# Kernel tuning notes

Measured on AMD Instinct MI355X. Metric: run time of the kernel, lower is better.

The kernel has to match this reference:

```python
import jax, jax.numpy as jnp
import numpy as np

EPS = 1e-5

def gru_step(x, h, Wih, Whh, bih, bhh):
    # PyTorch GRU cell math. x:[B,C], h:[B,H], Wih:[3H,C], Whh:[3H,H]
    gi = x @ Wih.T + bih
    gh = h @ Whh.T + bhh
    ir, iz, inn = jnp.split(gi, 3, axis=-1)
    hr, hz, hn = jnp.split(gh, 3, axis=-1)
    r = jax.nn.sigmoid(ir + hr)
    z = jax.nn.sigmoid(iz + hz)
    n = jnp.tanh(inn + r * hn)
    return (1.0 - z) * n + z * h

def batchnorm_train(x, g, b):
    # x:[B,C]; training-mode BN over batch dim, biased variance
    mu = jnp.mean(x, axis=0)
    var = jnp.mean((x - mu) ** 2, axis=0)
    return g * (x - mu) / jnp.sqrt(var + EPS) + b

def setup_inputs() -> dict:
    B, Le, T = 256, 1024, 48
    Fe, Fd, G, R, H = 16, 16, 32, 16, 256
    Ce, Cd = Fe + R, Fd + R + 1  # 32, 33
    key = jax.random.key(0)
    ks = jax.random.split(key, 24)
    s = 0.05
    inp = {
        "X_Encoder": jax.random.normal(ks[0], (B, Le, Fe), jnp.float32),
        "X_Decoder": jax.random.normal(ks[1], (B, T, Fd), jnp.float32),
        "Xg_Encoder": jax.random.normal(ks[2], (B, Le, G), jnp.float32),
        "Xg_Decoder": jax.random.normal(ks[3], (B, T, G), jnp.float32),
        # global feature reducers
        "Wg_enc": jax.random.normal(ks[4], (R, G), jnp.float32) * s,
        "bg_enc": jnp.zeros((R,), jnp.float32),
        "Wg_dec": jax.random.normal(ks[5], (R, G), jnp.float32) * s,
        "bg_dec": jnp.zeros((R,), jnp.float32),
        # encoder GRU + output head
        "enc_Wih": jax.random.normal(ks[6], (3 * H, Ce), jnp.float32) * s,
        "enc_Whh": jax.random.normal(ks[7], (3 * H, H), jnp.float32) * s,
        "enc_bih": jnp.zeros((3 * H,), jnp.float32),
        "enc_bhh": jnp.zeros((3 * H,), jnp.float32),
        "enc_Wo": jax.random.normal(ks[8], (1, H), jnp.float32) * s,
        "enc_bo": jnp.zeros((1,), jnp.float32),
        # decoder GRU + output head
        "dec_Wih": jax.random.normal(ks[9], (3 * H, Cd), jnp.float32) * s,
        "dec_Whh": jax.random.normal(ks[10], (3 * H, H), jnp.float32) * s,
        "dec_bih": jnp.zeros((3 * H,), jnp.float32),
        "dec_bhh": jnp.zeros((3 * H,), jnp.float32),
        "dec_Wo": jax.random.normal(ks[11], (1, H), jnp.float32) * s,
        "dec_bo": jnp.zeros((1,), jnp.float32),
        # BatchNorm params: BN_1 and per-step BN_layers (T of them)
        "bn1_g": jnp.ones((Cd,), jnp.float32),
        "bn1_b": jnp.zeros((Cd,), jnp.float32),
        "bnT_g": jnp.ones((T, Cd), jnp.float32),
        "bnT_b": jnp.zeros((T, Cd), jnp.float32),
    }
    return inp

def reference(X_Encoder, X_Decoder, Xg_Encoder, Xg_Decoder,
              Wg_enc, bg_enc, Wg_dec, bg_dec,
              enc_Wih, enc_Whh, enc_bih, enc_bhh, enc_Wo, enc_bo,
              dec_Wih, dec_Whh, dec_bih, dec_bhh, dec_Wo, dec_bo,
              bn1_g, bn1_b, bnT_g, bnT_b):
    B, Le, _ = X_Encoder.shape
    T = X_Decoder.shape[1]
    H = enc_Whh.shape[1]
    # batched global-feature reduction (replaces nested per-element loops)
    enc_in = jnp.concatenate([X_Encoder, Xg_Encoder @ Wg_enc.T + bg_enc], axis=2)  # [B,Le,Ce]
    dec_wg = jnp.concatenate([X_Decoder, Xg_Decoder @ Wg_dec.T + bg_dec], axis=2)  # [B,T,Fd+R]
    # encoder: sequential GRU over Le steps
    def estep(h, x):
        return gru_step(x, h, enc_Wih, enc_Whh, enc_bih, enc_bhh), None
    h0 = jnp.zeros((B, H), enc_in.dtype)
    h_enc, _ = jax.lax.scan(estep, h0, jnp.swapaxes(enc_in, 0, 1))
    enc_out = h_enc @ enc_Wo.T + enc_bo  # [B,1]
    # first decoder input: concat + BN_1 (train mode); dropout p=0 -> identity
    dec_in0 = batchnorm_train(jnp.concatenate([dec_wg[:, 0], enc_out], axis=1), bn1_g, bn1_b)
    # next-step exogenous inputs, padded with zeros for the (unused) last step
    next_x = jnp.concatenate([dec_wg[:, 1:], jnp.zeros((B, 1, dec_wg.shape[2]), dec_wg.dtype)], axis=1)
    next_x = jnp.swapaxes(next_x, 0, 1)  # [T,B,Fd+R]
    def dstep(carry, xs):
        h, dinp = carry
        nx, g, b = xs
        h = gru_step(dinp, h, dec_Wih, dec_Whh, dec_bih, dec_bhh)
        out = h @ dec_Wo.T + dec_bo  # [B,1]
        new_in = batchnorm_train(jnp.concatenate([nx, out], axis=1), g, b)
        return (h, new_in), out
    (_, _), outs = jax.lax.scan(dstep, (h_enc, dec_in0), (next_x, bnT_g, bnT_b))
    return jnp.swapaxes(outs, 0, 1)  # [B,T,1]
```

## Files before the change

### kernel.cpp

```cpp
#include <hip/hip_runtime.h>
#include <math.h>

typedef _Float16 f16;
typedef _Float16 f16x8 __attribute__((ext_vector_type(8)));
typedef float f32x4 __attribute__((ext_vector_type(4)));

#define MFMA16(A_, B_, C_) __builtin_amdgcn_mfma_f32_16x16x32_f16((A_), (B_), (C_), 0, 0, 0)

__device__ __forceinline__ float sigf(float x) { return 1.0f / (1.0f + __expf(-x)); }
__device__ __forceinline__ float tanhf_(float x) { float e = __expf(2.0f * x); return 1.0f - 2.0f / (e + 1.0f); }

static const size_t OFF_ENCIN = 0;
static const size_t OFF_DECIN = 16777216;
static const size_t OFF_WENC  = OFF_DECIN + 786432;
static const size_t OFF_WDEC  = OFF_WENC + 442368;
static const size_t OFF_W32   = OFF_WDEC + 442368;
static const size_t OFF_BE    = OFF_W32 + 3072;
static const size_t OFF_BD    = OFF_BE + 4096;
static const size_t OFF_HENC  = OFF_BD + 4096;
static const size_t OFF_EOUT  = OFF_HENC + 131072;
static const size_t OFF_XST   = OFF_EOUT + 1024;
static const size_t OFF_OST   = OFF_XST + 12288;
static const size_t OFF_BAR   = OFF_OST + 512;

struct P {
  const float *Xe, *Xd, *Xge, *Xgd, *Wge, *bge, *Wgd, *bgd;
  const float *eWih, *eWhh, *ebih, *ebhh, *eWo, *ebo;
  const float *dWih, *dWhh, *dbih, *dbhh, *dWo, *dbo;
  const float *bn1g, *bn1b, *bnTg, *bnTb;
  f16 *encin, *decin, *wencf, *wdecf;
  float *w32, *bE, *bD;
  f16 *henc;
  float *eout, *xst, *ost;
  int *bar;
  float *out;
};

__global__ void prep1(P p) {
  const int blk = blockIdx.x, tid = threadIdx.x;
  __shared__ float swg[512];
  __shared__ float sbg[16];
  if (blk < 1024) {
    for (int i = tid; i < 512; i += 256) swg[i] = p.Wge[i];
    if (tid < 16) sbg[tid] = p.bge[tid];
    __syncthreads();
    const int i = blk * 256 + tid;
    const int b = i >> 10, t = i & 1023;
    const float* xg = p.Xge + (size_t)(b * 1024 + t) * 32;
    const float* xe = p.Xe + (size_t)(b * 1024 + t) * 16;
    f16* o = p.encin + (size_t)(t * 256 + b) * 32;
    float xgv[32];
#pragma unroll
    for (int k = 0; k < 32; ++k) xgv[k] = xg[k];
#pragma unroll
    for (int c = 0; c < 16; ++c) o[c] = (f16)xe[c];
#pragma unroll 4
    for (int r = 0; r < 16; ++r) {
      float acc = sbg[r];
#pragma unroll
      for (int k = 0; k < 32; ++k) acc += swg[r * 32 + k] * xgv[k];
      o[16 + r] = (f16)acc;
    }
  } else if (blk < 1072) {
    for (int i = tid; i < 512; i += 256) swg[i] = p.Wgd[i];
    if (tid < 16) sbg[tid] = p.bgd[tid];
    __syncthreads();
    const int i = (blk - 1024) * 256 + tid;
    const int b = i / 48, t = i - b * 48;
    const float* xg = p.Xgd + (size_t)(b * 48 + t) * 32;
    const float* xd = p.Xd + (size_t)(b * 48 + t) * 16;
    f16* o = p.decin + (size_t)(t * 256 + b) * 32;
    float xgv[32];
#pragma unroll
    for (int k = 0; k < 32; ++k) xgv[k] = xg[k];
#pragma unroll
    for (int c = 0; c < 16; ++c) o[c] = (f16)xd[c];
#pragma unroll 4
    for (int r = 0; r < 16; ++r) {
      float acc = sbg[r];
#pragma unroll
      for (int k = 0; k < 32; ++k) acc += swg[r * 32 + k] * xgv[k];
      o[16 + r] = (f16)acc;
    }
  } else if (blk < 1180) {
    const int i = (blk - 1072) * 256 + tid;
    const int kt = i / 3072, r2 = i - kt * 3072;
    const int nt = r2 >> 6, l = r2 & 63;
    const int n = nt * 16 + (l & 15), g = l >> 4;
    f16* o = p.wencf + (size_t)i * 8;
#pragma unroll
    for (int j = 0; j < 8; ++j) {
      const int k = g * 8 + j;
      o[j] = (f16)((kt == 0) ? p.eWih[n * 32 + k] : p.eWhh[n * 256 + (kt - 1) * 32 + k]);
    }
  } else if (blk < 1288) {
    const int i = (blk - 1180) * 256 + tid;
    const int kt = i / 3072, r2 = i - kt * 3072;
    const int nt = r2 >> 6, l = r2 & 63;
    const int n = nt * 16 + (l & 15), g = l >> 4;
    f16* o = p.wdecf + (size_t)i * 8;
#pragma unroll
    for (int j = 0; j < 8; ++j) {
      const int k = g * 8 + j;
      o[j] = (f16)((kt == 0) ? p.dWih[n * 33 + k] : p.dWhh[n * 256 + (kt - 1) * 32 + k]);
    }
  } else if (blk == 1288) {
    for (int i = tid; i < 768; i += 256) p.w32[i] = p.dWih[i * 33 + 32];
    for (int i = tid; i < 96; i += 256) p.ost[i] = 0.f;
    if (tid == 0) { p.bar[0] = 0; p.bar[1] = 0; }
  } else if (blk == 1289) {
    for (int i = tid; i < 1024; i += 256) {
      float v;
      if (i < 512) v = p.ebih[i] + p.ebhh[i];
      else if (i < 768) v = p.ebih[i];
      else v = p.ebhh[i - 256];
      p.bE[i] = v;
    }
  } else {
    for (int i = tid; i < 1024; i += 256) {
      float v;
      if (i < 512) v = p.dbih[i] + p.dbhh[i];
      else if (i < 768) v = p.dbih[i];
      else v = p.dbhh[i - 256];
      p.bD[i] = v;
    }
  }
}

__global__ void prep2(P p) {
  const int i = blockIdx.x * 256 + threadIdx.x;
  if (i >= 48 * 32) return;
  const int s = i >> 5, c = i & 31;
  float s1 = 0.f, s2 = 0.f;
  for (int b = 0; b < 256; ++b) {
    const float v = (float)p.decin[(size_t)(s * 256 + b) * 32 + c];
    s1 += v; s2 += v * v;
  }
  const float mu = s1 * (1.0f / 256.0f);
  p.xst[i * 2] = mu;
  p.xst[i * 2 + 1] = s2 * (1.0f / 256.0f) - mu * mu;
}

__device__ __forceinline__ void gridbar(int* bar) {
  __syncthreads();
  if (threadIdx.x == 0) {
    const int g = __hip_atomic_load(&bar[1], __ATOMIC_ACQUIRE, __HIP_MEMORY_SCOPE_AGENT);
    const int a = __hip_atomic_fetch_add(&bar[0], 1, __ATOMIC_ACQ_REL, __HIP_MEMORY_SCOPE_AGENT);
    if (a == 15) {
      __hip_atomic_store(&bar[0], 0, __ATOMIC_RELAXED, __HIP_MEMORY_SCOPE_AGENT);
      __hip_atomic_store(&bar[1], g + 1, __ATOMIC_RELEASE, __HIP_MEMORY_SCOPE_AGENT);
    } else {
      while (__hip_atomic_load(&bar[1], __ATOMIC_ACQUIRE, __HIP_MEMORY_SCOPE_AGENT) == g) {
        __builtin_amdgcn_s_sleep(2);
      }
    }
  }
  __syncthreads();
}

__global__ __launch_bounds__(512, 2) void enc_kernel(P p) {
  __shared__ f16 sWL[49152];
  __shared__ f16 sH[8192];
  __shared__ float sRed[512];
  const int tid = threadIdx.x;
  const int l = tid & 63, w = tid >> 6;
  const int g = l >> 4, m16 = l & 15;
  const int sw16 = (m16 & 7) << 4;
  const int bg = blockIdx.x * 16;

  {
    const int4* src = (const int4*)(p.wencf + 172032);
    int4* dst = (int4*)sWL;
#pragma unroll
    for (int i = 0; i < 12; ++i) dst[tid + i * 512] = src[tid + i * 512];
  }
  {
    int* hz = (int*)sH;
#pragma unroll
    for (int i = 0; i < 8; ++i) hz[tid + i * 512] = 0;
  }
  const int nts[6] = {w, 8 + w, 16 + w, 24 + w, 32 + w, 40 + w};
  f16x8 Wr[7][6];
#pragma unroll
  for (int kt = 0; kt < 7; ++kt)
#pragma unroll
    for (int i = 0; i < 6; ++i)
      Wr[kt][i] = *(const f16x8*)(p.wencf + ((size_t)(kt * 48 + nts[i]) * 64 + l) * 8);
  const int J1 = 16 * w + m16, J2 = 128 + J1;
  const float br1 = p.bE[J1], bz1 = p.bE[256 + J1], bi1 = p.bE[512 + J1], bh1 = p.bE[768 + J1];
  const float br2 = p.bE[J2], bz2 = p.bE[256 + J2], bi2 = p.bE[512 + J2], bh2 = p.bE[768 + J2];
  __syncthreads();

  int ph = 0;
  f16x8 xf = *(const f16x8*)(p.encin + (size_t)(bg + m16) * 32 + 8 * g);
#pragma unroll 1
  for (int t = 0; t < 1024; ++t) {
    const int tn = (t < 1023) ? t + 1 : t;
    const f16x8 xn = *(const f16x8*)(p.encin + (size_t)(tn * 256 + bg + m16) * 32 + 8 * g);
    f32x4 aR0 = {0,0,0,0}, aR1 = {0,0,0,0}, aZ0 = {0,0,0,0}, aZ1 = {0,0,0,0};
    f32x4 aNi0 = {0,0,0,0}, aNi1 = {0,0,0,0}, aNh0 = {0,0,0,0}, aNh1 = {0,0,0,0};
    aR0 = MFMA16(xf, Wr[0][0], aR0);
    aR1 = MFMA16(xf, Wr[0][1], aR1);
    aZ0 = MFMA16(xf, Wr[0][2], aZ0);
    aZ1 = MFMA16(xf, Wr[0][3], aZ1);
    aNi0 = MFMA16(xf, Wr[0][4], aNi0);
    aNi1 = MFMA16(xf, Wr[0][5], aNi1);
#pragma unroll
    for (int kk = 1; kk <= 6; ++kk) {
      const f16x8 a = *(const f16x8*)((const char*)sH + ph * 8192 + m16 * 512 +
                                      ((64 * (kk - 1) + 16 * g) ^ sw16));
      aR0 = MFMA16(a, Wr[kk][0], aR0);
      aR1 = MFMA16(a, Wr[kk][1], aR1);
      aZ0 = MFMA16(a, Wr[kk][2], aZ0);
      aZ1 = MFMA16(a, Wr[kk][3], aZ1);
      aNh0 = MFMA16(a, Wr[kk][4], aNh0);
      aNh1 = MFMA16(a, Wr[kk][5], aNh1);
    }
#pragma unroll
    for (int kk = 7; kk <= 8; ++kk) {
      const f16x8 a = *(const f16x8*)((const char*)sH + ph * 8192 + m16 * 512 +
                                      ((64 * (kk - 1) + 16 * g) ^ sw16));
      const char* wb = (const char*)sWL + (kk - 7) * 49152;
      const f16x8 q0 = *(const f16x8*)(wb + (nts[0] * 64 + l) * 16);
      const f16x8 q1 = *(const f16x8*)(wb + (nts[1] * 64 + l) * 16);
      const f16x8 q2 = *(const f16x8*)(wb + (nts[2] * 64 + l) * 16);
      const f16x8 q3 = *(const f16x8*)(wb + (nts[3] * 64 + l) * 16);
      const f16x8 q4 = *(const f16x8*)(wb + (nts[4] * 64 + l) * 16);
      const f16x8 q5 = *(const f16x8*)(wb + (nts[5] * 64 + l) * 16);
      aR0 = MFMA16(a, q0, aR0);
      aR1 = MFMA16(a, q1, aR1);
      aZ0 = MFMA16(a, q2, aZ0);
      aZ1 = MFMA16(a, q3, aZ1);
      aNh0 = MFMA16(a, q4, aNh0);
      aNh1 = MFMA16(a, q5, aNh1);
    }
    {
      char* hw = (char*)sH + (ph ^ 1) * 8192;
      const char* hr = (const char*)sH + ph * 8192;
#pragma unroll
      for (int q = 0; q < 4; ++q) {
        const int m = 4 * g + q;
        const int sw = (m & 7) << 4;
        const float h1 = (float)*(const f16*)(hr + m * 512 + ((2 * J1) ^ sw));
        const float r1 = sigf(aR0[q] + br1);
        const float z1 = sigf(aZ0[q] + bz1);
        const float n1 = tanhf_(aNi0[q] + bi1 + r1 * (aNh0[q] + bh1));
        *(f16*)(hw + m * 512 + ((2 * J1) ^ sw)) = (f16)((1.0f - z1) * n1 + z1 * h1);
        const float h2 = (float)*(const f16*)(hr + m * 512 + ((2 * J2) ^ sw));
        const float r2 = sigf(aR1[q] + br2);
        const float z2 = sigf(aZ1[q] + bz2);
        const float n2 = tanhf_(aNi1[q] + bi2 + r2 * (aNh1[q] + bh2));
        *(f16*)(hw + m * 512 + ((2 * J2) ^ sw)) = (f16)((1.0f - z2) * n2 + z2 * h2);
      }
    }
    __syncthreads();
    ph ^= 1;
    xf = xn;
  }
  {
    const char* hb = (const char*)sH + ph * 8192;
    const int m = tid & 15, grp = tid >> 4;
    const f16x8 hv = *(const f16x8*)(hb + m * 512 + ((16 * grp) ^ ((m & 7) << 4)));
    *(f16x8*)(p.henc + (size_t)(bg + m) * 256 + 8 * grp) = hv;
    float part = 0.f;
#pragma unroll
    for (int jj = 0; jj < 8; ++jj) part += (float)hv[jj] * p.eWo[8 * grp + jj];
    sRed[m * 32 + grp] = part;
    __syncthreads();
    if (tid < 16) {
      float o = p.ebo[0];
#pragma unroll 8
      for (int k = 0; k < 32; ++k) o += sRed[tid * 32 + k];
      p.eout[bg + tid] = o;
    }
  }
}

__global__ __launch_bounds__(512, 2) void dec_kernel(P p) {
  __shared__ f16 sWL[49152];
  __shared__ f16 sH[8192];
  __shared__ f16 sDin[1024];
  __shared__ float sRed[512];
  __shared__ float sOutv[16];
  __shared__ float sO32[16];
  const int tid = threadIdx.x;
  const int l = tid & 63, w = tid >> 6;
  const int g = l >> 4, m16 = l & 15;
  const int sw16 = (m16 & 7) << 4;
  const int bg = blockIdx.x * 16;

  {
    const int4* src = (const int4*)(p.wdecf + 172032);
    int4* dst = (int4*)sWL;
#pragma unroll
    for (int i = 0; i < 12; ++i) dst[tid + i * 512] = src[tid + i * 512];
  }
  {
    const int m = tid & 15, grp = tid >> 4;
    const f16x8 hv = *(const f16x8*)(p.henc + (size_t)(bg + m) * 256 + 8 * grp);
    *(f16x8*)((char*)sH + m * 512 + ((16 * grp) ^ ((m & 7) << 4))) = hv;
  }
  if (tid < 128) ((int4*)sDin)[tid] = int4{0, 0, 0, 0};
  const int nts[6] = {w, 8 + w, 16 + w, 24 + w, 32 + w, 40 + w};
  f16x8 Wr[7][6];
#pragma unroll
  for (int kt = 0; kt < 7; ++kt)
#pragma unroll
    for (int i = 0; i < 6; ++i)
      Wr[kt][i] = *(const f16x8*)(p.wdecf + ((size_t)(kt * 48 + nts[i]) * 64 + l) * 8);
  const int J1 = 16 * w + m16, J2 = 128 + J1;
  const float br1 = p.bD[J1], bz1 = p.bD[256 + J1], bi1 = p.bD[512 + J1], bh1 = p.bD[768 + J1];
  const float br2 = p.bD[J2], bz2 = p.bD[256 + J2], bi2 = p.bD[512 + J2], bh2 = p.bD[768 + J2];
  const float w32r1 = p.w32[J1], w32z1 = p.w32[256 + J1], w32n1 = p.w32[512 + J1];
  const float w32r2 = p.w32[J2], w32z2 = p.w32[256 + J2], w32n2 = p.w32[512 + J2];
  __syncthreads();

  {
    if (tid < 16) sOutv[tid] = p.eout[bg + tid];
    __syncthreads();
    if (tid == 0) {
      float s1 = 0.f, s2 = 0.f;
#pragma unroll
      for (int k = 0; k < 16; ++k) { const float v = sOutv[k]; s1 += v; s2 += v * v; }
      atomicAdd(&p.ost[0], s1);
      atomicAdd(&p.ost[1], s2);
    }
    gridbar(p.bar);
    if (tid < 16) {
      const float S1 = __hip_atomic_load(&p.ost[0], __ATOMIC_RELAXED, __HIP_MEMORY_SCOPE_AGENT);
      const float S2 = __hip_atomic_load(&p.ost[1], __ATOMIC_RELAXED, __HIP_MEMORY_SCOPE_AGENT);
      const float mu = S1 * (1.0f / 256.0f);
      const float var = S2 * (1.0f / 256.0f) - mu * mu;
      sO32[tid] = p.bn1g[32] * (sOutv[tid] - mu) / sqrtf(var + 1e-5f) + p.bn1b[32];
    }
    {
      const int m = tid & 15, c = tid >> 4;
      const float x = (float)p.decin[(size_t)(bg + m) * 32 + c];
      const float mx = p.xst[c * 2], vx = p.xst[c * 2 + 1];
      const float v = p.bn1g[c] * (x - mx) / sqrtf(vx + 1e-5f) + p.bn1b[c];
      *(f16*)((char*)sDin + m * 128 + ((2 * c) ^ ((m & 7) << 4))) = (f16)v;
    }
    __syncthreads();
  }

  int ph = 0;
#pragma unroll 1
  for (int t = 0; t < 48; ++t) {
    f32x4 aR0 = {0,0,0,0}, aR1 = {0,0,0,0}, aZ0 = {0,0,0,0}, aZ1 = {0,0,0,0};
    f32x4 aNi0 = {0,0,0,0}, aNi1 = {0,0,0,0}, aNh0 = {0,0,0,0}, aNh1 = {0,0,0,0};
    {
      const f16x8 a = *(const f16x8*)((const char*)sDin + m16 * 128 + ((16 * g) ^ sw16));
      aR0 = MFMA16(a, Wr[0][0], aR0);
      aR1 = MFMA16(a, Wr[0][1], aR1);
      aZ0 = MFMA16(a, Wr[0][2], aZ0);
      aZ1 = MFMA16(a, Wr[0][3], aZ1);
      aNi0 = MFMA16(a, Wr[0][4], aNi0);
      aNi1 = MFMA16(a, Wr[0][5], aNi1);
    }
#pragma unroll
    for (int kk = 1; kk <= 6; ++kk) {
      const f16x8 a = *(const f16x8*)((const char*)sH + ph * 8192 + m16 * 512 +
                                      ((64 * (kk - 1) + 16 * g) ^ sw16));
      aR0 = MFMA16(a, Wr[kk][0], aR0);
      aR1 = MFMA16(a, Wr[kk][1], aR1);
      aZ0 = MFMA16(a, Wr[kk][2], aZ0);
      aZ1 = MFMA16(a, Wr[kk][3], aZ1);
      aNh0 = MFMA16(a, Wr[kk][4], aNh0);
      aNh1 = MFMA16(a, Wr[kk][5], aNh1);
    }
#pragma unroll
    for (int kk = 7; kk <= 8; ++kk) {
      const f16x8 a = *(const f16x8*)((const char*)sH + ph * 8192 + m16 * 512 +
                                      ((64 * (kk - 1) + 16 * g) ^ sw16));
      const char* wb = (const char*)sWL + (kk - 7) * 49152;
      const f16x8 q0 = *(const f16x8*)(wb + (nts[0] * 64 + l) * 16);
      const f16x8 q1 = *(const f16x8*)(wb + (nts[1] * 64 + l) * 16);
      const f16x8 q2 = *(const f16x8*)(wb + (nts[2] * 64 + l) * 16);
      const f16x8 q3 = *(const f16x8*)(wb + (nts[3] * 64 + l) * 16);
      const f16x8 q4 = *(const f16x8*)(wb + (nts[4] * 64 + l) * 16);
      const f16x8 q5 = *(const f16x8*)(wb + (nts[5] * 64 + l) * 16);
      aR0 = MFMA16(a, q0, aR0);
      aR1 = MFMA16(a, q1, aR1);
      aZ0 = MFMA16(a, q2, aZ0);
      aZ1 = MFMA16(a, q3, aZ1);
      aNh0 = MFMA16(a, q4, aNh0);
      aNh1 = MFMA16(a, q5, aNh1);
    }
    {
      char* hw = (char*)sH + (ph ^ 1) * 8192;
      const char* hr = (const char*)sH + ph * 8192;
#pragma unroll
      for (int q = 0; q < 4; ++q) {
        const int m = 4 * g + q;
        const int sw = (m & 7) << 4;
        const float o32m = sO32[m];
        const float h1 = (float)*(const f16*)(hr + m * 512 + ((2 * J1) ^ sw));
        const float r1 = sigf(aR0[q] + br1 + o32m * w32r1);
        const float z1 = sigf(aZ0[q] + bz1 + o32m * w32z1);
        const float n1 = tanhf_(aNi0[q] + bi1 + o32m * w32n1 + r1 * (aNh0[q] + bh1));
        *(f16*)(hw + m * 512 + ((2 * J1) ^ sw)) = (f16)((1.0f - z1) * n1 + z1 * h1);
        const float h2 = (float)*(const f16*)(hr + m * 512 + ((2 * J2) ^ sw));
        const float r2 = sigf(aR1[q] + br2 + o32m * w32r2);
        const float z2 = sigf(aZ1[q] + bz2 + o32m * w32z2);
        const float n2 = tanhf_(aNi1[q] + bi2 + o32m * w32n2 + r2 * (aNh1[q] + bh2));
        *(f16*)(hw + m * 512 + ((2 * J2) ^ sw)) = (f16)((1.0f - z2) * n2 + z2 * h2);
      }
    }
    __syncthreads();
    {
      const int m = tid & 15, grp = tid >> 4;
      const char* hb = (const char*)sH + (ph ^ 1) * 8192;
      const f16x8 hv = *(const f16x8*)(hb + m * 512 + ((16 * grp) ^ ((m & 7) << 4)));
      float part = 0.f;
#pragma unroll
      for (int jj = 0; jj < 8; ++jj) part += (float)hv[jj] * p.dWo[8 * grp + jj];
      sRed[m * 32 + grp] = part;
    }
    __syncthreads();
    if (tid < 16) {
      float o = p.dbo[0];
#pragma unroll 8
      for (int k = 0; k < 32; ++k) o += sRed[tid * 32 + k];
      p.out[(size_t)(bg + tid) * 48 + t] = o;
      sOutv[tid] = o;
    }
    if (t < 47) {
      __syncthreads();
      if (tid == 0) {
        float s1 = 0.f, s2 = 0.f;
#pragma unroll
        for (int k = 0; k < 16; ++k) { const float v = sOutv[k]; s1 += v; s2 += v * v; }
        atomicAdd(&p.ost[(t + 1) * 2 + 0], s1);
        atomicAdd(&p.ost[(t + 1) * 2 + 1], s2);
      }
      gridbar(p.bar);
      if (tid < 16) {
        const float S1 = __hip_atomic_load(&p.ost[(t + 1) * 2 + 0], __ATOMIC_RELAXED, __HIP_MEMORY_SCOPE_AGENT);
        const float S2 = __hip_atomic_load(&p.ost[(t + 1) * 2 + 1], __ATOMIC_RELAXED, __HIP_MEMORY_SCOPE_AGENT);
        const float mu = S1 * (1.0f / 256.0f);
        const float var = S2 * (1.0f / 256.0f) - mu * mu;
        sO32[tid] = p.bnTg[t * 33 + 32] * (sOutv[tid] - mu) / sqrtf(var + 1e-5f) + p.bnTb[t * 33 + 32];
      }
      {
        const int m = tid & 15, c = tid >> 4;
        const int s = t + 1;
        const float x = (float)p.decin[(size_t)(s * 256 + bg + m) * 32 + c];
        const float mx = p.xst[(s * 32 + c) * 2], vx = p.xst[(s * 32 + c) * 2 + 1];
        const float v = p.bnTg[t * 33 + c] * (x - mx) / sqrtf(vx + 1e-5f) + p.bnTb[t * 33 + c];
        *(f16*)((char*)sDin + m * 128 + ((2 * c) ^ ((m & 7) << 4))) = (f16)v;
      }
      __syncthreads();
    }
    ph ^= 1;
  }
}

extern "C" void kernel_launch(void* const* d_in, const int* in_sizes, int n_in,
                              void* d_out, int out_size, void* d_ws, size_t ws_size,
                              hipStream_t stream) {
  char* ws = (char*)d_ws;
  P p;
  p.Xe   = (const float*)d_in[0];
  p.Xd   = (const float*)d_in[1];
  p.Xge  = (const float*)d_in[2];
  p.Xgd  = (const float*)d_in[3];
  p.Wge  = (const float*)d_in[4];
  p.bge  = (const float*)d_in[5];
  p.Wgd  = (const float*)d_in[6];
  p.bgd  = (const float*)d_in[7];
  p.eWih = (const float*)d_in[8];
  p.eWhh = (const float*)d_in[9];
  p.ebih = (const float*)d_in[10];
  p.ebhh = (const float*)d_in[11];
  p.eWo  = (const float*)d_in[12];
  p.ebo  = (const float*)d_in[13];
  p.dWih = (const float*)d_in[14];
  p.dWhh = (const float*)d_in[15];
  p.dbih = (const float*)d_in[16];
  p.dbhh = (const float*)d_in[17];
  p.dWo  = (const float*)d_in[18];
  p.dbo  = (const float*)d_in[19];
  p.bn1g = (const float*)d_in[20];
  p.bn1b = (const float*)d_in[21];
  p.bnTg = (const float*)d_in[22];
  p.bnTb = (const float*)d_in[23];
  p.encin = (f16*)(ws + OFF_ENCIN);
  p.decin = (f16*)(ws + OFF_DECIN);
  p.wencf = (f16*)(ws + OFF_WENC);
  p.wdecf = (f16*)(ws + OFF_WDEC);
  p.w32   = (float*)(ws + OFF_W32);
  p.bE    = (float*)(ws + OFF_BE);
  p.bD    = (float*)(ws + OFF_BD);
  p.henc  = (f16*)(ws + OFF_HENC);
  p.eout  = (float*)(ws + OFF_EOUT);
  p.xst   = (float*)(ws + OFF_XST);
  p.ost   = (float*)(ws + OFF_OST);
  p.bar   = (int*)(ws + OFF_BAR);
  p.out   = (float*)d_out;

  prep1<<<dim3(1291), dim3(256), 0, stream>>>(p);
  prep2<<<dim3(6), dim3(256), 0, stream>>>(p);
  enc_kernel<<<dim3(16), dim3(512), 0, stream>>>(p);
  dec_kernel<<<dim3(16), dim3(512), 0, stream>>>(p);
}
```

Before: 3.330 ms.

## Replace decoder grid barrier with per-step counters and overlap hidden GEMM with wait

The decoder's full grid barrier is replaced by per-timestep arrival counters, so each block computes the recurrent h·Whh MFMAs before waiting for the batch-norm statistics of the previous output. The input-side MFMA then runs after the wait. The change also folds biases into accumulator initialisation, keeps the previous hidden state in registers instead of re-reading LDS, uses hardware rcp/rsq, and changes the LDS swizzle. It depends on the counter array being zeroed by the prep kernel, and the approximate reciprocals slightly change numerics.

```diff
diff --git a/kernel.cpp b/kernel.cpp
--- a/kernel.cpp
+++ b/kernel.cpp
@@ -6,9 +6,12 @@
 typedef float f32x4 __attribute__((ext_vector_type(4)));
 
 #define MFMA16(A_, B_, C_) __builtin_amdgcn_mfma_f32_16x16x32_f16((A_), (B_), (C_), 0, 0, 0)
-
-__device__ __forceinline__ float sigf(float x) { return 1.0f / (1.0f + __expf(-x)); }
-__device__ __forceinline__ float tanhf_(float x) { float e = __expf(2.0f * x); return 1.0f - 2.0f / (e + 1.0f); }
+#define SWZ(m) ((((m) & 7) ^ (((m) & 8) >> 2)) << 4)
+
+__device__ __forceinline__ float rcpf_(float x) { return __builtin_amdgcn_rcpf(x); }
+__device__ __forceinline__ float rsqf_(float x) { return __builtin_amdgcn_rsqf(x); }
+__device__ __forceinline__ float sigf(float x) { return rcpf_(1.0f + __expf(-x)); }
+__device__ __forceinline__ float tanhf_(float x) { return 1.0f - 2.0f * rcpf_(__expf(2.0f * x) + 1.0f); }
 
 static const size_t OFF_ENCIN = 0;
 static const size_t OFF_DECIN = 16777216;
@@ -21,7 +24,7 @@
 static const size_t OFF_EOUT  = OFF_HENC + 131072;
 static const size_t OFF_XST   = OFF_EOUT + 1024;
 static const size_t OFF_OST   = OFF_XST + 12288;
-static const size_t OFF_BAR   = OFF_OST + 512;
+static const size_t OFF_CNT   = OFF_OST + 512;
 
 struct P {
   const float *Xe, *Xd, *Xge, *Xgd, *Wge, *bge, *Wgd, *bgd;
@@ -32,7 +35,7 @@
   float *w32, *bE, *bD;
   f16 *henc;
   float *eout, *xst, *ost;
-  int *bar;
+  int *cnt;
   float *out;
 };
 
@@ -106,8 +109,8 @@
     }
   } else if (blk == 1288) {
     for (int i = tid; i < 768; i += 256) p.w32[i] = p.dWih[i * 33 + 32];
-    for (int i = tid; i < 96; i += 256) p.ost[i] = 0.f;
-    if (tid == 0) { p.bar[0] = 0; p.bar[1] = 0; }
+    for (int i = tid; i < 128; i += 256) p.ost[i] = 0.f;
+    if (tid < 64) p.cnt[tid] = 0;
   } else if (blk == 1289) {
     for (int i = tid; i < 1024; i += 256) {
       float v;
@@ -141,23 +144,6 @@
   p.xst[i * 2 + 1] = s2 * (1.0f / 256.0f) - mu * mu;
 }
 
-__device__ __forceinline__ void gridbar(int* bar) {
-  __syncthreads();
-  if (threadIdx.x == 0) {
-    const int g = __hip_atomic_load(&bar[1], __ATOMIC_ACQUIRE, __HIP_MEMORY_SCOPE_AGENT);
-    const int a = __hip_atomic_fetch_add(&bar[0], 1, __ATOMIC_ACQ_REL, __HIP_MEMORY_SCOPE_AGENT);
-    if (a == 15) {
-      __hip_atomic_store(&bar[0], 0, __ATOMIC_RELAXED, __HIP_MEMORY_SCOPE_AGENT);
-      __hip_atomic_store(&bar[1], g + 1, __ATOMIC_RELEASE, __HIP_MEMORY_SCOPE_AGENT);
-    } else {
-      while (__hip_atomic_load(&bar[1], __ATOMIC_ACQUIRE, __HIP_MEMORY_SCOPE_AGENT) == g) {
-        __builtin_amdgcn_s_sleep(2);
-      }
-    }
-  }
-  __syncthreads();
-}
-
 __global__ __launch_bounds__(512, 2) void enc_kernel(P p) {
   __shared__ f16 sWL[49152];
   __shared__ f16 sH[8192];
@@ -165,7 +151,7 @@
   const int tid = threadIdx.x;
   const int l = tid & 63, w = tid >> 6;
   const int g = l >> 4, m16 = l & 15;
-  const int sw16 = (m16 & 7) << 4;
+  const int swzA = SWZ(m16);
   const int bg = blockIdx.x * 16;
 
   {
@@ -189,6 +175,7 @@
   const int J1 = 16 * w + m16, J2 = 128 + J1;
   const float br1 = p.bE[J1], bz1 = p.bE[256 + J1], bi1 = p.bE[512 + J1], bh1 = p.bE[768 + J1];
   const float br2 = p.bE[J2], bz2 = p.bE[256 + J2], bi2 = p.bE[512 + J2], bh2 = p.bE[768 + J2];
+  float hp1[4] = {0.f, 0.f, 0.f, 0.f}, hp2[4] = {0.f, 0.f, 0.f, 0.f};
   __syncthreads();
 
   int ph = 0;
@@ -197,8 +184,10 @@
   for (int t = 0; t < 1024; ++t) {
     const int tn = (t < 1023) ? t + 1 : t;
     const f16x8 xn = *(const f16x8*)(p.encin + (size_t)(tn * 256 + bg + m16) * 32 + 8 * g);
-    f32x4 aR0 = {0,0,0,0}, aR1 = {0,0,0,0}, aZ0 = {0,0,0,0}, aZ1 = {0,0,0,0};
-    f32x4 aNi0 = {0,0,0,0}, aNi1 = {0,0,0,0}, aNh0 = {0,0,0,0}, aNh1 = {0,0,0,0};
+    f32x4 aR0 = {br1, br1, br1, br1}, aR1 = {br2, br2, br2, br2};
+    f32x4 aZ0 = {bz1, bz1, bz1, bz1}, aZ1 = {bz2, bz2, bz2, bz2};
+    f32x4 aNi0 = {bi1, bi1, bi1, bi1}, aNi1 = {bi2, bi2, bi2, bi2};
+    f32x4 aNh0 = {bh1, bh1, bh1, bh1}, aNh1 = {bh2, bh2, bh2, bh2};
     aR0 = MFMA16(xf, Wr[0][0], aR0);
     aR1 = MFMA16(xf, Wr[0][1], aR1);
     aZ0 = MFMA16(xf, Wr[0][2], aZ0);
@@ -208,7 +197,7 @@
 #pragma unroll
     for (int kk = 1; kk <= 6; ++kk) {
       const f16x8 a = *(const f16x8*)((const char*)sH + ph * 8192 + m16 * 512 +
-                                      ((64 * (kk - 1) + 16 * g) ^ sw16));
+                                      ((64 * (kk - 1) + 16 * g) ^ swzA));
       aR0 = MFMA16(a, Wr[kk][0], aR0);
       aR1 = MFMA16(a, Wr[kk][1], aR1);
       aZ0 = MFMA16(a, Wr[kk][2], aZ0);
@@ -219,7 +208,7 @@
 #pragma unroll
     for (int kk = 7; kk <= 8; ++kk) {
       const f16x8 a = *(const f16x8*)((const char*)sH + ph * 8192 + m16 * 512 +
-                                      ((64 * (kk - 1) + 16 * g) ^ sw16));
+                                      ((64 * (kk - 1) + 16 * g) ^ swzA));
       const char* wb = (const char*)sWL + (kk - 7) * 49152;
       const f16x8 q0 = *(const f16x8*)(wb + (nts[0] * 64 + l) * 16);
       const f16x8 q1 = *(const f16x8*)(wb + (nts[1] * 64 + l) * 16);
@@ -236,21 +225,22 @@
     }
     {
       char* hw = (char*)sH + (ph ^ 1) * 8192;
-      const char* hr = (const char*)sH + ph * 8192;
 #pragma unroll
       for (int q = 0; q < 4; ++q) {
         const int m = 4 * g + q;
-        const int sw = (m & 7) << 4;
-        const float h1 = (float)*(const f16*)(hr + m * 512 + ((2 * J1) ^ sw));
-        const float r1 = sigf(aR0[q] + br1);
-        const float z1 = sigf(aZ0[q] + bz1);
-        const float n1 = tanhf_(aNi0[q] + bi1 + r1 * (aNh0[q] + bh1));
-        *(f16*)(hw + m * 512 + ((2 * J1) ^ sw)) = (f16)((1.0f - z1) * n1 + z1 * h1);
-        const float h2 = (float)*(const f16*)(hr + m * 512 + ((2 * J2) ^ sw));
-        const float r2 = sigf(aR1[q] + br2);
-        const float z2 = sigf(aZ1[q] + bz2);
-        const float n2 = tanhf_(aNi1[q] + bi2 + r2 * (aNh1[q] + bh2));
-        *(f16*)(hw + m * 512 + ((2 * J2) ^ sw)) = (f16)((1.0f - z2) * n2 + z2 * h2);
+        const int sw = SWZ(m);
+        const float r1 = sigf(aR0[q]);
+        const float z1 = sigf(aZ0[q]);
+        const float n1 = tanhf_(aNi0[q] + r1 * aNh0[q]);
+        const f16 h1 = (f16)(n1 + z1 * (hp1[q] - n1));
+        hp1[q] = (float)h1;
+        *(f16*)(hw + m * 512 + ((2 * J1) ^ sw)) = h1;
+        const float r2 = sigf(aR1[q]);
+        const float z2 = sigf(aZ1[q]);
+        const float n2 = tanhf_(aNi1[q] + r2 * aNh1[q]);
+        const f16 h2 = (f16)(n2 + z2 * (hp2[q] - n2));
+        hp2[q] = (float)h2;
+        *(f16*)(hw + m * 512 + ((2 * J2) ^ sw)) = h2;
       }
     }
     __syncthreads();
@@ -260,7 +250,7 @@
   {
     const char* hb = (const char*)sH + ph * 8192;
     const int m = tid & 15, grp = tid >> 4;
-    const f16x8 hv = *(const f16x8*)(hb + m * 512 + ((16 * grp) ^ ((m & 7) << 4)));
+    const f16x8 hv = *(const f16x8*)(hb + m * 512 + ((16 * grp) ^ SWZ(m)));
     *(f16x8*)(p.henc + (size_t)(bg + m) * 256 + 8 * grp) = hv;
     float part = 0.f;
 #pragma unroll
@@ -287,6 +277,7 @@
   const int l = tid & 63, w = tid >> 6;
   const int g = l >> 4, m16 = l & 15;
   const int sw16 = (m16 & 7) << 4;
+  const int swzA = SWZ(m16);
   const int bg = blockIdx.x * 16;
 
   {
@@ -298,7 +289,7 @@
   {
     const int m = tid & 15, grp = tid >> 4;
     const f16x8 hv = *(const f16x8*)(p.henc + (size_t)(bg + m) * 256 + 8 * grp);
-    *(f16x8*)((char*)sH + m * 512 + ((16 * grp) ^ ((m & 7) << 4))) = hv;
+    *(f16x8*)((char*)sH + m * 512 + ((16 * grp) ^ SWZ(m))) = hv;
   }
   if (tid < 128) ((int4*)sDin)[tid] = int4{0, 0, 0, 0};
   const int nts[6] = {w, 8 + w, 16 + w, 24 + w, 32 + w, 40 + w};
@@ -313,54 +304,44 @@
   const float br2 = p.bD[J2], bz2 = p.bD[256 + J2], bi2 = p.bD[512 + J2], bh2 = p.bD[768 + J2];
   const float w32r1 = p.w32[J1], w32z1 = p.w32[256 + J1], w32n1 = p.w32[512 + J1];
   const float w32r2 = p.w32[J2], w32z2 = p.w32[256 + J2], w32n2 = p.w32[512 + J2];
+  float hp1[4], hp2[4];
+#pragma unroll
+  for (int q = 0; q < 4; ++q) {
+    hp1[q] = (float)p.henc[(size_t)(bg + 4 * g + q) * 256 + J1];
+    hp2[q] = (float)p.henc[(size_t)(bg + 4 * g + q) * 256 + J2];
+  }
+  if (tid < 16) sOutv[tid] = p.eout[bg + tid];
   __syncthreads();
-
-  {
-    if (tid < 16) sOutv[tid] = p.eout[bg + tid];
-    __syncthreads();
-    if (tid == 0) {
-      float s1 = 0.f, s2 = 0.f;
-#pragma unroll
-      for (int k = 0; k < 16; ++k) { const float v = sOutv[k]; s1 += v; s2 += v * v; }
-      atomicAdd(&p.ost[0], s1);
-      atomicAdd(&p.ost[1], s2);
-    }
-    gridbar(p.bar);
-    if (tid < 16) {
-      const float S1 = __hip_atomic_load(&p.ost[0], __ATOMIC_RELAXED, __HIP_MEMORY_SCOPE_AGENT);
-      const float S2 = __hip_atomic_load(&p.ost[1], __ATOMIC_RELAXED, __HIP_MEMORY_SCOPE_AGENT);
-      const float mu = S1 * (1.0f / 256.0f);
-      const float var = S2 * (1.0f / 256.0f) - mu * mu;
-      sO32[tid] = p.bn1g[32] * (sOutv[tid] - mu) / sqrtf(var + 1e-5f) + p.bn1b[32];
-    }
-    {
-      const int m = tid & 15, c = tid >> 4;
-      const float x = (float)p.decin[(size_t)(bg + m) * 32 + c];
-      const float mx = p.xst[c * 2], vx = p.xst[c * 2 + 1];
-      const float v = p.bn1g[c] * (x - mx) / sqrtf(vx + 1e-5f) + p.bn1b[c];
-      *(f16*)((char*)sDin + m * 128 + ((2 * c) ^ ((m & 7) << 4))) = (f16)v;
-    }
-    __syncthreads();
+  if (tid == 0) {
+    float s1 = 0.f, s2 = 0.f;
+#pragma unroll
+    for (int k = 0; k < 16; ++k) { const float v = sOutv[k]; s1 += v; s2 += v * v; }
+    atomicAdd(&p.ost[0], s1);
+    atomicAdd(&p.ost[1], s2);
+    __hip_atomic_fetch_add(&p.cnt[0], 1, __ATOMIC_RELEASE, __HIP_MEMORY_SCOPE_AGENT);
   }
 
   int ph = 0;
 #pragma unroll 1
   for (int t = 0; t < 48; ++t) {
-    f32x4 aR0 = {0,0,0,0}, aR1 = {0,0,0,0}, aZ0 = {0,0,0,0}, aZ1 = {0,0,0,0};
-    f32x4 aNi0 = {0,0,0,0}, aNi1 = {0,0,0,0}, aNh0 = {0,0,0,0}, aNh1 = {0,0,0,0};
-    {
-      const f16x8 a = *(const f16x8*)((const char*)sDin + m16 * 128 + ((16 * g) ^ sw16));
-      aR0 = MFMA16(a, Wr[0][0], aR0);
-      aR1 = MFMA16(a, Wr[0][1], aR1);
-      aZ0 = MFMA16(a, Wr[0][2], aZ0);
-      aZ1 = MFMA16(a, Wr[0][3], aZ1);
-      aNi0 = MFMA16(a, Wr[0][4], aNi0);
-      aNi1 = MFMA16(a, Wr[0][5], aNi1);
-    }
+    const int mp = tid & 15, cp = tid >> 4;
+    const float xq = (float)p.decin[((size_t)t * 256 + bg + mp) * 32 + cp];
+    const float mx = p.xst[(t * 32 + cp) * 2], vx = p.xst[(t * 32 + cp) * 2 + 1];
+    const float gc = (t == 0) ? p.bn1g[cp] : p.bnTg[(t - 1) * 33 + cp];
+    const float bc = (t == 0) ? p.bn1b[cp] : p.bnTb[(t - 1) * 33 + cp];
+    float gK = 0.f, bK = 0.f;
+    if (tid < 16) {
+      gK = (t == 0) ? p.bn1g[32] : p.bnTg[(t - 1) * 33 + 32];
+      bK = (t == 0) ? p.bn1b[32] : p.bnTb[(t - 1) * 33 + 32];
+    }
+    f32x4 aR0 = {br1, br1, br1, br1}, aR1 = {br2, br2, br2, br2};
+    f32x4 aZ0 = {bz1, bz1, bz1, bz1}, aZ1 = {bz2, bz2, bz2, bz2};
+    f32x4 aNi0 = {bi1, bi1, bi1, bi1}, aNi1 = {bi2, bi2, bi2, bi2};
+    f32x4 aNh0 = {bh1, bh1, bh1, bh1}, aNh1 = {bh2, bh2, bh2, bh2};
 #pragma unroll
     for (int kk = 1; kk <= 6; ++kk) {
       const f16x8 a = *(const f16x8*)((const char*)sH + ph * 8192 + m16 * 512 +
-                                      ((64 * (kk - 1) + 16 * g) ^ sw16));
+                                      ((64 * (kk - 1) + 16 * g) ^ swzA));
       aR0 = MFMA16(a, Wr[kk][0], aR0);
       aR1 = MFMA16(a, Wr[kk][1], aR1);
       aZ0 = MFMA16(a, Wr[kk][2], aZ0);
@@ -371,7 +352,7 @@
 #pragma unroll
     for (int kk = 7; kk <= 8; ++kk) {
       const f16x8 a = *(const f16x8*)((const char*)sH + ph * 8192 + m16 * 512 +
-                                      ((64 * (kk - 1) + 16 * g) ^ sw16));
+                                      ((64 * (kk - 1) + 16 * g) ^ swzA));
       const char* wb = (const char*)sWL + (kk - 7) * 49152;
       const f16x8 q0 = *(const f16x8*)(wb + (nts[0] * 64 + l) * 16);
       const f16x8 q1 = *(const f16x8*)(wb + (nts[1] * 64 + l) * 16);
@@ -386,31 +367,56 @@
       aNh0 = MFMA16(a, q4, aNh0);
       aNh1 = MFMA16(a, q5, aNh1);
     }
+    if (tid == 0) {
+      while (__hip_atomic_load(&p.cnt[t], __ATOMIC_ACQUIRE, __HIP_MEMORY_SCOPE_AGENT) < 16)
+        __builtin_amdgcn_s_sleep(1);
+    }
+    __syncthreads();
+    if (tid < 16) {
+      const float S1 = __hip_atomic_load(&p.ost[2 * t], __ATOMIC_RELAXED, __HIP_MEMORY_SCOPE_AGENT);
+      const float S2 = __hip_atomic_load(&p.ost[2 * t + 1], __ATOMIC_RELAXED, __HIP_MEMORY_SCOPE_AGENT);
+      const float mu = S1 * (1.0f / 256.0f);
+      const float var = S2 * (1.0f / 256.0f) - mu * mu;
+      sO32[tid] = gK * (sOutv[tid] - mu) * rsqf_(var + 1e-5f) + bK;
+    }
+    *(f16*)((char*)sDin + mp * 128 + ((2 * cp) ^ ((mp & 7) << 4))) =
+        (f16)(gc * (xq - mx) * rsqf_(vx + 1e-5f) + bc);
+    __syncthreads();
+    {
+      const f16x8 a = *(const f16x8*)((const char*)sDin + m16 * 128 + ((16 * g) ^ sw16));
+      aR0 = MFMA16(a, Wr[0][0], aR0);
+      aR1 = MFMA16(a, Wr[0][1], aR1);
+      aZ0 = MFMA16(a, Wr[0][2], aZ0);
+      aZ1 = MFMA16(a, Wr[0][3], aZ1);
+      aNi0 = MFMA16(a, Wr[0][4], aNi0);
+      aNi1 = MFMA16(a, Wr[0][5], aNi1);
+    }
     {
       char* hw = (char*)sH + (ph ^ 1) * 8192;
-      const char* hr = (const char*)sH + ph * 8192;
 #pragma unroll
       for (int q = 0; q < 4; ++q) {
         const int m = 4 * g + q;
-        const int sw = (m & 7) << 4;
+        const int sw = SWZ(m);
         const float o32m = sO32[m];
-        const float h1 = (float)*(const f16*)(hr + m * 512 + ((2 * J1) ^ sw));
-        const float r1 = sigf(aR0[q] + br1 + o32m * w32r1);
-        const float z1 = sigf(aZ0[q] + bz1 + o32m * w32z1);
-        const float n1 = tanhf_(aNi0[q] + bi1 + o32m * w32n1 + r1 * (aNh0[q] + bh1));
-        *(f16*)(hw + m * 512 + ((2 * J1) ^ sw)) = (f16)((1.0f - z1) * n1 + z1 * h1);
-        const float h2 = (float)*(const f16*)(hr + m * 512 + ((2 * J2) ^ sw));
-        const float r2 = sigf(aR1[q] + br2 + o32m * w32r2);
-        const float z2 = sigf(aZ1[q] + bz2 + o32m * w32z2);
-        const float n2 = tanhf_(aNi1[q] + bi2 + o32m * w32n2 + r2 * (aNh1[q] + bh2));
-        *(f16*)(hw + m * 512 + ((2 * J2) ^ sw)) = (f16)((1.0f - z2) * n2 + z2 * h2);
+        const float r1 = sigf(aR0[q] + o32m * w32r1);
+        const float z1 = sigf(aZ0[q] + o32m * w32z1);
+        const float n1 = tanhf_(aNi0[q] + o32m * w32n1 + r1 * aNh0[q]);
+        const f16 h1 = (f16)(n1 + z1 * (hp1[q] - n1));
+        hp1[q] = (float)h1;
+        *(f16*)(hw + m * 512 + ((2 * J1) ^ sw)) = h1;
+        const float r2 = sigf(aR1[q] + o32m * w32r2);
+        const float z2 = sigf(aZ1[q] + o32m * w32z2);
+        const float n2 = tanhf_(aNi1[q] + o32m * w32n2 + r2 * aNh1[q]);
+        const f16 h2 = (f16)(n2 + z2 * (hp2[q] - n2));
+        hp2[q] = (float)h2;
+        *(f16*)(hw + m * 512 + ((2 * J2) ^ sw)) = h2;
       }
     }
     __syncthreads();
     {
       const int m = tid & 15, grp = tid >> 4;
       const char* hb = (const char*)sH + (ph ^ 1) * 8192;
-      const f16x8 hv = *(const f16x8*)(hb + m * 512 + ((16 * grp) ^ ((m & 7) << 4)));
+      const f16x8 hv = *(const f16x8*)(hb + m * 512 + ((16 * grp) ^ SWZ(m)));
       float part = 0.f;
 #pragma unroll
       for (int jj = 0; jj < 8; ++jj) part += (float)hv[jj] * p.dWo[8 * grp + jj];
@@ -424,32 +430,14 @@
       p.out[(size_t)(bg + tid) * 48 + t] = o;
       sOutv[tid] = o;
     }
-    if (t < 47) {
-      __syncthreads();
-      if (tid == 0) {
-        float s1 = 0.f, s2 = 0.f;
-#pragma unroll
-        for (int k = 0; k < 16; ++k) { const float v = sOutv[k]; s1 += v; s2 += v * v; }
-        atomicAdd(&p.ost[(t + 1) * 2 + 0], s1);
-        atomicAdd(&p.ost[(t + 1) * 2 + 1], s2);
-      }
-      gridbar(p.bar);
-      if (tid < 16) {
-        const float S1 = __hip_atomic_load(&p.ost[(t + 1) * 2 + 0], __ATOMIC_RELAXED, __HIP_MEMORY_SCOPE_AGENT);
-        const float S2 = __hip_atomic_load(&p.ost[(t + 1) * 2 + 1], __ATOMIC_RELAXED, __HIP_MEMORY_SCOPE_AGENT);
-        const float mu = S1 * (1.0f / 256.0f);
-        const float var = S2 * (1.0f / 256.0f) - mu * mu;
-        sO32[tid] = p.bnTg[t * 33 + 32] * (sOutv[tid] - mu) / sqrtf(var + 1e-5f) + p.bnTb[t * 33 + 32];
-      }
-      {
-        const int m = tid & 15, c = tid >> 4;
-        const int s = t + 1;
-        const float x = (float)p.decin[(size_t)(s * 256 + bg + m) * 32 + c];
-        const float mx = p.xst[(s * 32 + c) * 2], vx = p.xst[(s * 32 + c) * 2 + 1];
-        const float v = p.bnTg[t * 33 + c] * (x - mx) / sqrtf(vx + 1e-5f) + p.bnTb[t * 33 + c];
-        *(f16*)((char*)sDin + m * 128 + ((2 * c) ^ ((m & 7) << 4))) = (f16)v;
-      }
-      __syncthreads();
+    __syncthreads();
+    if (t < 47 && tid == 0) {
+      float s1 = 0.f, s2 = 0.f;
+#pragma unroll
+      for (int k = 0; k < 16; ++k) { const float v = sOutv[k]; s1 += v; s2 += v * v; }
+      atomicAdd(&p.ost[2 * (t + 1)], s1);
+      atomicAdd(&p.ost[2 * (t + 1) + 1], s2);
+      __hip_atomic_fetch_add(&p.cnt[t + 1], 1, __ATOMIC_RELEASE, __HIP_MEMORY_SCOPE_AGENT);
     }
     ph ^= 1;
   }
@@ -495,7 +483,7 @@
   p.eout  = (float*)(ws + OFF_EOUT);
   p.xst   = (float*)(ws + OFF_XST);
   p.ost   = (float*)(ws + OFF_OST);
-  p.bar   = (int*)(ws + OFF_BAR);
+  p.cnt   = (int*)(ws + OFF_CNT);
   p.out   = (float*)d_out;
 
   prep1<<<dim3(1291), dim3(256), 0, stream>>>(p);
```

Measured after the change: 3.677 ms. 1.1x slower.
